# Kernel tuning notes

Measured on AMD Instinct MI355X. Metric: run time of the kernel, lower is better.

The kernel has to match this reference:

```python
import jax, jax.numpy as jnp
import numpy as np

B, K, D_MODEL = 64, 256, 512
D_STATE, D_CONV, EXPAND = 16, 4, 1
D_INNER = EXPAND * D_MODEL
DT_RANK = (D_MODEL + 15) // 16  # 32
EPS = 1e-5


def _layer_norm(x, g, b):
    m = jnp.mean(x, axis=-1, keepdims=True)
    v = jnp.mean(jnp.square(x - m), axis=-1, keepdims=True)
    return (x - m) * jax.lax.rsqrt(v + EPS) * g + b


def _silu(x):
    return x * jax.nn.sigmoid(x)


def _mamba_block(x, in_proj_w, conv_w, conv_b, x_proj_w, dt_proj_w, dt_proj_b, A_log, Dp, out_proj_w):
    # x: (B, K, d_model)
    b, k, _ = x.shape
    d_inner = A_log.shape[0]
    d_state = A_log.shape[1]
    dt_rank = dt_proj_w.shape[1]
    xz = x @ in_proj_w.T                      # (B, K, 2*d_inner)
    xi, z = jnp.split(xz, 2, axis=-1)
    # causal depthwise conv1d, width d_conv
    pad = conv_w.shape[1] - 1
    xp = jnp.pad(xi, ((0, 0), (pad, 0), (0, 0)))
    xc = conv_b + sum(xp[:, w:w + k, :] * conv_w[:, w] for w in range(conv_w.shape[1]))
    xc = _silu(xc)
    proj = xc @ x_proj_w.T                    # (B, K, dt_rank + 2*d_state)
    dtr = proj[..., :dt_rank]
    Bc = proj[..., dt_rank:dt_rank + d_state]  # (B, K, d_state)
    Cc = proj[..., dt_rank + d_state:]         # (B, K, d_state)
    dt = jax.nn.softplus(dtr @ dt_proj_w.T + dt_proj_b)  # (B, K, d_inner)
    A = -jnp.exp(A_log)                       # (d_inner, d_state)

    def step(h, inp):
        dt_t, x_t, B_t, C_t = inp             # (B,d_inner),(B,d_inner),(B,d_state),(B,d_state)
        dA = jnp.exp(dt_t[:, :, None] * A)    # (B, d_inner, d_state)
        h = dA * h + (dt_t * x_t)[:, :, None] * B_t[:, None, :]
        y = jnp.einsum('bds,bs->bd', h, C_t)
        return h, y

    h0 = jnp.zeros((b, d_inner, d_state), x.dtype)
    xs = (dt.transpose(1, 0, 2), xc.transpose(1, 0, 2),
          Bc.transpose(1, 0, 2), Cc.transpose(1, 0, 2))
    _, ys = jax.lax.scan(step, h0, xs)        # ys: (K, B, d_inner)
    y = ys.transpose(1, 0, 2) + xc * Dp       # skip term D*x
    y = y * _silu(z)
    return y @ out_proj_w.T


def setup_inputs() -> dict:
    key = jax.random.key(0)
    ks = jax.random.split(key, 8)
    s = 0.02
    slots = jax.random.normal(ks[0], (B, K, D_MODEL), dtype=jnp.float32)
    in_proj_w = jax.random.normal(ks[1], (2 * D_INNER, D_MODEL), jnp.float32) * s
    conv_w = jax.random.normal(ks[2], (D_INNER, D_CONV), jnp.float32) * 0.1
    conv_b = jnp.zeros((D_INNER,), jnp.float32)
    x_proj_w = jax.random.normal(ks[3], (DT_RANK + 2 * D_STATE, D_INNER), jnp.float32) * s
    dt_proj_w = jax.random.normal(ks[4], (D_INNER, DT_RANK), jnp.float32) * s
    dt_proj_b = jax.random.normal(ks[5], (D_INNER,), jnp.float32) * 0.1 - 4.0  # small softplus(dt)
    A_log = jnp.log(jnp.broadcast_to(jnp.arange(1, D_STATE + 1, dtype=jnp.float32), (D_INNER, D_STATE)))
    Dp = jnp.ones((D_INNER,), jnp.float32)
    out_proj_w = jax.random.normal(ks[6], (D_MODEL, D_INNER), jnp.float32) * s
    ln_g = jnp.ones((D_MODEL,), jnp.float32)
    ln_b = jnp.zeros((D_MODEL,), jnp.float32)
    fln_g = jnp.ones((D_MODEL,), jnp.float32)
    fln_b = jnp.zeros((D_MODEL,), jnp.float32)
    return {"slots": slots, "ln_g": ln_g, "ln_b": ln_b,
            "in_proj_w": in_proj_w, "conv_w": conv_w, "conv_b": conv_b,
            "x_proj_w": x_proj_w, "dt_proj_w": dt_proj_w, "dt_proj_b": dt_proj_b,
            "A_log": A_log, "Dp": Dp, "out_proj_w": out_proj_w,
            "fln_g": fln_g, "fln_b": fln_b}


def reference(slots, ln_g, ln_b, in_proj_w, conv_w, conv_b, x_proj_w,
              dt_proj_w, dt_proj_b, A_log, Dp, out_proj_w, fln_g, fln_b):
    x = slots
    # num_layers = 1: pre-norm -> mamba -> residual
    residual = x
    x = _layer_norm(x, ln_g, ln_b)
    x = _mamba_block(x, in_proj_w, conv_w, conv_b, x_proj_w,
                     dt_proj_w, dt_proj_b, A_log, Dp, out_proj_w)
    x = x + residual
    return _layer_norm(x, fln_g, fln_b)
```

## Files before the change

### kernel.cpp

```cpp
#include <hip/hip_runtime.h>
#include <hip/hip_bf16.h>


#define NTOK 16384
#define DM   512

typedef __attribute__((ext_vector_type(8))) short bf16x8;
typedef __attribute__((ext_vector_type(4))) float f32x4;

__device__ __forceinline__ unsigned short f2bf(float f){
  unsigned int u = __float_as_uint(f);
  u = (u + 0x7fffu + ((u >> 16) & 1u)) >> 16;
  return (unsigned short)u;
}
__device__ __forceinline__ float bfu(unsigned short p){ return __uint_as_float(((unsigned int)p) << 16); }
__device__ __forceinline__ unsigned int pk2(float a, float b){
  return (unsigned int)f2bf(a) | ((unsigned int)f2bf(b) << 16);
}
__device__ __forceinline__ float silu(float a){ return a / (1.f + __expf(-a)); }

__device__ __forceinline__ float qsum(float x){
  x += __int_as_float(__builtin_amdgcn_mov_dpp(__float_as_int(x), 0xB1, 0xF, 0xF, true));
  x += __int_as_float(__builtin_amdgcn_mov_dpp(__float_as_int(x), 0x4E, 0xF, 0xF, true));
  return x;
}

__device__ __forceinline__ void async_cp16(const unsigned short* g, unsigned short* l){
  __builtin_amdgcn_global_load_lds(
      (const __attribute__((address_space(1))) unsigned int*)g,
      (__attribute__((address_space(3))) unsigned int*)l, 16, 0, 0);
}

__global__ __launch_bounds__(256) void k_cvtw(const float* __restrict__ W,
                                              unsigned short* __restrict__ Wb){
  int i = (blockIdx.x*256 + threadIdx.x)*8;
  float4 a = *(const float4*)(W+i);
  float4 b = *(const float4*)(W+i+4);
  uint4 st = { pk2(a.x,a.y), pk2(a.z,a.w), pk2(b.x,b.y), pk2(b.z,b.w) };
  *(uint4*)(Wb+i) = st;
}

__global__ __launch_bounds__(64) void k_ln(const float* __restrict__ x,
                                           const float* __restrict__ g,
                                           const float* __restrict__ b,
                                           unsigned short* __restrict__ out){
  int tok  = blockIdx.x;
  int lane = threadIdx.x;
  const float* row = x + (size_t)tok*DM + lane*8;
  float4 r0 = *(const float4*)row;
  float4 r1 = *(const float4*)(row + 4);
  float v[8] = {r0.x,r0.y,r0.z,r0.w, r1.x,r1.y,r1.z,r1.w};
  float s = 0.f;
  #pragma unroll
  for (int i=0;i<8;i++) s += v[i];
  #pragma unroll
  for (int o=32;o;o>>=1) s += __shfl_xor(s, o, 64);
  float m = s * (1.0f/512.0f);
  float vs = 0.f;
  #pragma unroll
  for (int i=0;i<8;i++){ float d = v[i]-m; vs += d*d; }
  #pragma unroll
  for (int o=32;o;o>>=1) vs += __shfl_xor(vs, o, 64);
  float rs = rsqrtf(vs*(1.0f/512.0f) + 1e-5f);
  float4 g0 = *(const float4*)(g + lane*8);
  float4 g1 = *(const float4*)(g + lane*8 + 4);
  float4 b0 = *(const float4*)(b + lane*8);
  float4 b1 = *(const float4*)(b + lane*8 + 4);
  float gv[8] = {g0.x,g0.y,g0.z,g0.w, g1.x,g1.y,g1.z,g1.w};
  float bv[8] = {b0.x,b0.y,b0.z,b0.w, b1.x,b1.y,b1.z,b1.w};
  float o8[8];
  #pragma unroll
  for (int i=0;i<8;i++) o8[i] = (v[i]-m)*rs*gv[i] + bv[i];
  uint4 st = { pk2(o8[0],o8[1]), pk2(o8[2],o8[3]), pk2(o8[4],o8[5]), pk2(o8[6],o8[7]) };
  *(uint4*)(out + (size_t)tok*DM + lane*8) = st;
}

__global__ __launch_bounds__(256) void k_gemm(const unsigned short* __restrict__ A,
                                              const unsigned short* __restrict__ Wb,
                                              float* __restrict__ out_f,
                                              unsigned short* __restrict__ out_b,
                                              unsigned short* __restrict__ out_x,
                                              int mode){
  __shared__ unsigned short As[2][128*32];
  __shared__ unsigned short Bs[2][128*32];
  int t0  = blockIdx.x * 128;
  int n0  = blockIdx.y * 128;
  int tid = threadIdx.x;
  int lane = tid & 63;
  int wv  = tid >> 6;
  int mw  = wv & 1, nw = wv >> 1;
  int m15 = lane & 15, quad = lane >> 4;

  int srow   = wv*32 + (lane >> 2);
  int schunk = ((lane & 3) ^ ((lane >> 3) & 3)) * 8;
  const unsigned short* gA = A  + (size_t)(t0 + srow)*DM + schunk;
  const unsigned short* gB = Wb + (size_t)(n0 + srow)*DM + schunk;
  unsigned short* asb0 = &As[0][(wv*32)*32];
  unsigned short* bsb0 = &Bs[0][(wv*32)*32];
  unsigned short* asb1 = &As[1][(wv*32)*32];
  unsigned short* bsb1 = &Bs[1][(wv*32)*32];

  async_cp16(gA,         asb0);
  async_cp16(gA + 16*DM, asb0 + 16*32);
  async_cp16(gB,         bsb0);
  async_cp16(gB + 16*DM, bsb0 + 16*32);

  f32x4 acc[4][4];
  #pragma unroll
  for (int rb=0;rb<4;rb++)
    #pragma unroll
    for (int cb=0;cb<4;cb++) acc[rb][cb] = (f32x4){0.f,0.f,0.f,0.f};

  int rdsw = (quad ^ ((m15 >> 1) & 3)) * 8;
  int cur = 0;
  for (int ks = 0; ks < 16; ks++){
    __syncthreads();
    if (ks < 15){
      const unsigned short* nA = gA + (ks+1)*32;
      const unsigned short* nB = gB + (ks+1)*32;
      unsigned short* na = cur ? asb0 : asb1;
      unsigned short* nb = cur ? bsb0 : bsb1;
      async_cp16(nA,         na);
      async_cp16(nA + 16*DM, na + 16*32);
      async_cp16(nB,         nb);
      async_cp16(nB + 16*DM, nb + 16*32);
    }
    bf16x8 af[4], bfr[4];
    #pragma unroll
    for (int rb=0;rb<4;rb++)
      af[rb] = *(const bf16x8*)&As[cur][(mw*64 + rb*16 + m15)*32 + rdsw];
    #pragma unroll
    for (int cb=0;cb<4;cb++)
      bfr[cb] = *(const bf16x8*)&Bs[cur][(nw*64 + cb*16 + m15)*32 + rdsw];
    #pragma unroll
    for (int rb=0;rb<4;rb++)
      #pragma unroll
      for (int cb=0;cb<4;cb++)
        acc[rb][cb] = __builtin_amdgcn_mfma_f32_16x16x32_bf16(af[rb], bfr[cb], acc[rb][cb], 0, 0, 0);
    cur ^= 1;
  }

  #pragma unroll
  for (int rb=0;rb<4;rb++){
    int tok0 = t0 + mw*64 + rb*16 + quad*4;
    int b    = tok0 >> 8;
    int tl0  = tok0 & 255;
    #pragma unroll
    for (int cb=0;cb<4;cb++){
      int nn = n0 + nw*64 + cb*16 + m15;
      f32x4 v = acc[rb][cb];
      if (mode == 0){
        if (nn < DM){
          *(uint2*)(out_x + ((size_t)(b*DM + nn))*256 + tl0)
              = (uint2){ pk2(v[0],v[1]), pk2(v[2],v[3]) };
        } else {
          *(uint2*)(out_b + ((size_t)(b*DM + (nn - DM)))*256 + tl0)
              = (uint2){ pk2(silu(v[0]), silu(v[1])), pk2(silu(v[2]), silu(v[3])) };
        }
      } else {
        #pragma unroll
        for (int r=0;r<4;r++) out_f[(size_t)(tok0+r)*DM + nn] = v[r];
      }
    }
  }
}

__global__ __launch_bounds__(256) void k_xproj(const unsigned short* __restrict__ xiTb,
                                               const float* __restrict__ cw,
                                               const float* __restrict__ cb,
                                               const unsigned short* __restrict__ xpwb,
                                               const unsigned short* __restrict__ dtwb,
                                               const float* __restrict__ dtb,
                                               unsigned short* __restrict__ dtTb,
                                               unsigned short* __restrict__ xcT,
                                               float* __restrict__ Bc,
                                               float* __restrict__ Cc){
  __shared__ unsigned short xcb[16*520];
  __shared__ unsigned short pjA[16*40];
  int t0  = blockIdx.x * 16;
  int b   = t0 >> 8;
  int tl0 = t0 & 255;
  int tid = threadIdx.x;
  int lane = tid & 63;
  int wv  = tid >> 6;
  int m15 = lane & 15, quad = lane >> 4;

  #pragma unroll
  for (int j=0;j<2;j++){
    int d = tid + 256*j;
    float4 cr = *(const float4*)(cw + d*4);
    float a0 = cb[d];
    const unsigned short* row = xiTb + ((size_t)(b*DM + d))*256;
    float w[20];
    if (tl0 == 0){
      w[0]=w[1]=w[2]=w[3]=0.f;
      #pragma unroll
      for (int q2=0;q2<4;q2++){
        uint2 v2 = *(const uint2*)(row + q2*4);
        w[4+q2*4+0]=bfu((unsigned short)v2.x);
        w[4+q2*4+1]=bfu((unsigned short)(v2.x>>16));
        w[4+q2*4+2]=bfu((unsigned short)v2.y);
        w[4+q2*4+3]=bfu((unsigned short)(v2.y>>16));
      }
    } else {
      const unsigned short* p = row + tl0 - 4;
      #pragma unroll
      for (int q2=0;q2<5;q2++){
        uint2 v2 = *(const uint2*)(p + q2*4);
        w[q2*4+0]=bfu((unsigned short)v2.x);
        w[q2*4+1]=bfu((unsigned short)(v2.x>>16));
        w[q2*4+2]=bfu((unsigned short)v2.y);
        w[q2*4+3]=bfu((unsigned short)(v2.y>>16));
      }
    }
    unsigned int pkv[8];
    #pragma unroll
    for (int t=0;t<16;t+=2){
      float s0 = silu(a0 + w[t+1]*cr.x + w[t+2]*cr.y + w[t+3]*cr.z + w[t+4]*cr.w);
      float s1 = silu(a0 + w[t+2]*cr.x + w[t+3]*cr.y + w[t+4]*cr.z + w[t+5]*cr.w);
      unsigned int pp = pk2(s0, s1);
      xcb[t*520 + d]     = (unsigned short)pp;
      xcb[(t+1)*520 + d] = (unsigned short)(pp >> 16);
      pkv[t>>1] = pp;
    }
    unsigned short* xr = xcT + ((size_t)(b*DM + d))*256 + tl0;
    *(uint4*)(xr)     = (uint4){ pkv[0], pkv[1], pkv[2], pkv[3] };
    *(uint4*)(xr + 8) = (uint4){ pkv[4], pkv[5], pkv[6], pkv[7] };
  }
  __syncthreads();

  f32x4 pacc = (f32x4){0.f,0.f,0.f,0.f};
  #pragma unroll 4
  for (int ks=0; ks<16; ks++){
    bf16x8 af  = *(const bf16x8*)&xcb[m15*520 + ks*32 + quad*8];
    bf16x8 bfr = *(const bf16x8*)(xpwb + (size_t)(wv*16 + m15)*DM + ks*32 + quad*8);
    pacc = __builtin_amdgcn_mfma_f32_16x16x32_bf16(af, bfr, pacc, 0, 0, 0);
  }

  if (wv < 2){
    #pragma unroll
    for (int r=0;r<4;r++)
      pjA[(quad*4 + r)*40 + wv*16 + m15] = f2bf(pacc[r]);
  } else if (wv == 2){
    #pragma unroll
    for (int r=0;r<4;r++)
      Bc[(size_t)(t0 + quad*4 + r)*16 + m15] = pacc[r];
  } else {
    #pragma unroll
    for (int r=0;r<4;r++)
      Cc[(size_t)(t0 + quad*4 + r)*16 + m15] = pacc[r];
  }
  __syncthreads();

  bf16x8 adt = *(const bf16x8*)&pjA[m15*40 + quad*8];
  #pragma unroll
  for (int j2=0;j2<8;j2++){
    int nn = (wv*8 + j2)*16 + m15;
    bf16x8 bfr = *(const bf16x8*)(dtwb + nn*32 + quad*8);
    f32x4 dacc = (f32x4){0.f,0.f,0.f,0.f};
    dacc = __builtin_amdgcn_mfma_f32_16x16x32_bf16(adt, bfr, dacc, 0, 0, 0);
    float bb = dtb[nn];
    float s0 = dacc[0] + bb, s1 = dacc[1] + bb, s2 = dacc[2] + bb, s3 = dacc[3] + bb;
    float o0 = (s0 > 20.f) ? s0 : log1pf(__expf(s0));
    float o1 = (s1 > 20.f) ? s1 : log1pf(__expf(s1));
    float o2 = (s2 > 20.f) ? s2 : log1pf(__expf(s2));
    float o3 = (s3 > 20.f) ? s3 : log1pf(__expf(s3));
    *(uint2*)(dtTb + ((size_t)(b*DM + nn))*256 + tl0 + quad*4)
        = (uint2){ pk2(o0,o1), pk2(o2,o3) };
  }
}

#define SCAN_STEP(DV, UV, BV, CV, ZS, OUT) do {                                 \
    float dv_ = (DV);                                                           \
    float u_  = (UV);                                                           \
    float du_ = dv_*u_;                                                         \
    h0 = fmaf(exp2f(dv_*A0), h0, du_*(BV).x);                                   \
    h1 = fmaf(exp2f(dv_*A1), h1, du_*(BV).y);                                   \
    h2 = fmaf(exp2f(dv_*A2), h2, du_*(BV).z);                                   \
    h3 = fmaf(exp2f(dv_*A3), h3, du_*(BV).w);                                   \
    float yy_ = fmaf(h3,(CV).w, fmaf(h2,(CV).z, fmaf(h1,(CV).y, h0*(CV).x)));   \
    yy_ = qsum(yy_);                                                            \
    OUT = fmaf(u_, Dv, yy_) * (ZS);                                             \
  } while(0)

#define SCAN_LOAD(DD, UU, ZZ, B0,B1,B2,B3, C0,C1,C2,C3) do {                    \
    DD  = *(const uint2*)dtp;  UU = *(const uint2*)xup;                         \
    ZZ  = *(const uint2*)zsp;                                                   \
    B0 = *(const float4*)(Bp);    B1 = *(const float4*)(Bp+16);                 \
    B2 = *(const float4*)(Bp+32); B3 = *(const float4*)(Bp+48);                 \
    C0 = *(const float4*)(Cp);    C1 = *(const float4*)(Cp+16);                 \
    C2 = *(const float4*)(Cp+32); C3 = *(const float4*)(Cp+48);                 \
    dtp += 4; xup += 4; zsp += 4; Bp += 64; Cp += 64;                           \
  } while(0)

#define SCAN_BODY(DD, UU, ZZ, B0,B1,B2,B3, C0,C1,C2,C3) do {                    \
    float dv0_ = __uint_as_float((DD).x << 16);                                 \
    float dv1_ = __uint_as_float((DD).x & 0xffff0000u);                         \
    float dv2_ = __uint_as_float((DD).y << 16);                                 \
    float dv3_ = __uint_as_float((DD).y & 0xffff0000u);                         \
    float u0_ = __uint_as_float((UU).x << 16);                                  \
    float u1_ = __uint_as_float((UU).x & 0xffff0000u);                          \
    float u2_ = __uint_as_float((UU).y << 16);                                  \
    float u3_ = __uint_as_float((UU).y & 0xffff0000u);                          \
    float zs0_ = __uint_as_float((ZZ).x << 16);                                 \
    float zs1_ = __uint_as_float((ZZ).x & 0xffff0000u);                         \
    float zs2_ = __uint_as_float((ZZ).y << 16);                                 \
    float zs3_ = __uint_as_float((ZZ).y & 0xffff0000u);                         \
    float o0_,o1_,o2_,o3_;                                                      \
    SCAN_STEP(dv0_,u0_,B0,C0,zs0_,o0_);                                         \
    SCAN_STEP(dv1_,u1_,B1,C1,zs1_,o1_);                                         \
    SCAN_STEP(dv2_,u2_,B2,C2,zs2_,o2_);                                         \
    SCAN_STEP(dv3_,u3_,B3,C3,zs3_,o3_);                                         \
    float osel_ = (sl==0)?o0_:(sl==1)?o1_:(sl==2)?o2_:o3_;                      \
    *yo = f2bf(osel_);                                                          \
    yo += 4*DM;                                                                 \
  } while(0)

__global__ __launch_bounds__(256) void k_scan(const unsigned short* __restrict__ dtT,
                                              const unsigned short* __restrict__ xcT,
                                              const unsigned short* __restrict__ zsT,
                                              const float* __restrict__ Bc,
                                              const float* __restrict__ Cc,
                                              const float* __restrict__ Alog,
                                              const float* __restrict__ Dpw,
                                              unsigned short* __restrict__ ya){
  int tid = threadIdx.x;
  int sl  = tid & 3;
  int q   = blockIdx.x*64 + (tid >> 2);
  int d   = q & 511;
  int b   = q >> 9;
  const float LOG2E = 1.44269504f;
  float4 Alr = *(const float4*)(Alog + d*16 + sl*4);
  float A0 = -__expf(Alr.x)*LOG2E, A1 = -__expf(Alr.y)*LOG2E;
  float A2 = -__expf(Alr.z)*LOG2E, A3 = -__expf(Alr.w)*LOG2E;
  float Dv = Dpw[d];
  float h0=0.f, h1=0.f, h2=0.f, h3=0.f;
  const unsigned short* dtp = dtT + (size_t)q*256;
  const unsigned short* xup = xcT + (size_t)q*256;
  const unsigned short* zsp = zsT + (size_t)q*256;
  unsigned short* yo = ya + (size_t)b*256*DM + d + sl*DM;
  const float* Bp = Bc + (size_t)b*4096 + sl*4;
  const float* Cp = Cc + (size_t)b*4096 + sl*4;

  uint2 ddA, uuA, zzA; float4 a0,a1,a2,a3, e0,e1,e2,e3;
  uint2 ddB, uuB, zzB; float4 f0,f1,f2,f3, g0,g1,g2,g3;

  SCAN_LOAD(ddA,uuA,zzA, a0,a1,a2,a3, e0,e1,e2,e3);
  for (int it = 0; it < 64; it += 2){
    SCAN_LOAD(ddB,uuB,zzB, f0,f1,f2,f3, g0,g1,g2,g3);
    SCAN_BODY(ddA,uuA,zzA, a0,a1,a2,a3, e0,e1,e2,e3);
    if (it < 62)
      SCAN_LOAD(ddA,uuA,zzA, a0,a1,a2,a3, e0,e1,e2,e3);
    SCAN_BODY(ddB,uuB,zzB, f0,f1,f2,f3, g0,g1,g2,g3);
  }
}

__global__ __launch_bounds__(64) void k_fln(const float* __restrict__ o,
                                            const float* __restrict__ resid,
                                            const float* __restrict__ g,
                                            const float* __restrict__ b,
                                            float* __restrict__ out){
  int tok  = blockIdx.x;
  int lane = threadIdx.x;
  const float* row = o     + (size_t)tok*DM + lane*8;
  const float* rr  = resid + (size_t)tok*DM + lane*8;
  float4 r0 = *(const float4*)row;
  float4 r1 = *(const float4*)(row + 4);
  float4 s0 = *(const float4*)rr;
  float4 s1 = *(const float4*)(rr + 4);
  float v[8] = {r0.x+s0.x, r0.y+s0.y, r0.z+s0.z, r0.w+s0.w,
                r1.x+s1.x, r1.y+s1.y, r1.z+s1.z, r1.w+s1.w};
  float s = 0.f;
  #pragma unroll
  for (int i=0;i<8;i++) s += v[i];
  #pragma unroll
  for (int o2=32;o2;o2>>=1) s += __shfl_xor(s, o2, 64);
  float m = s * (1.0f/512.0f);
  float vs = 0.f;
  #pragma unroll
  for (int i=0;i<8;i++){ float d = v[i]-m; vs += d*d; }
  #pragma unroll
  for (int o2=32;o2;o2>>=1) vs += __shfl_xor(vs, o2, 64);
  float rs = rsqrtf(vs*(1.0f/512.0f) + 1e-5f);
  float4 g0 = *(const float4*)(g + lane*8);
  float4 g1 = *(const float4*)(g + lane*8 + 4);
  float4 b0 = *(const float4*)(b + lane*8);
  float4 b1 = *(const float4*)(b + lane*8 + 4);
  float gv[8] = {g0.x,g0.y,g0.z,g0.w, g1.x,g1.y,g1.z,g1.w};
  float bv[8] = {b0.x,b0.y,b0.z,b0.w, b1.x,b1.y,b1.z,b1.w};
  float o8[8];
  #pragma unroll
  for (int i=0;i<8;i++) o8[i] = (v[i]-m)*rs*gv[i] + bv[i];
  float4* op = (float4*)(out + (size_t)tok*DM + lane*8);
  op[0] = make_float4(o8[0],o8[1],o8[2],o8[3]);
  op[1] = make_float4(o8[4],o8[5],o8[6],o8[7]);
}

extern "C" void kernel_launch(void* const* d_in, const int* in_sizes, int n_in,
                              void* d_out, int out_size, void* d_ws, size_t ws_size,
                              hipStream_t stream) {
  const float* slots     = (const float*)d_in[0];
  const float* ln_g      = (const float*)d_in[1];
  const float* ln_b      = (const float*)d_in[2];
  const float* in_proj_w = (const float*)d_in[3];
  const float* conv_w    = (const float*)d_in[4];
  const float* conv_b    = (const float*)d_in[5];
  const float* x_proj_w  = (const float*)d_in[6];
  const float* dt_proj_w = (const float*)d_in[7];
  const float* dt_proj_b = (const float*)d_in[8];
  const float* A_log     = (const float*)d_in[9];
  const float* Dp        = (const float*)d_in[10];
  const float* out_projw = (const float*)d_in[11];
  const float* fln_g     = (const float*)d_in[12];
  const float* fln_b     = (const float*)d_in[13];
  float* out = (float*)d_out;

  const size_t MB = 1024*1024;
  char* base = (char*)d_ws;
  unsigned short* xiTb = (unsigned short*)(base);
  unsigned short* xlnb = (unsigned short*)(base + 32*MB);
  unsigned short* yab  = xlnb;
  unsigned short* xpwb = xlnb;
  unsigned short* dtwb = xlnb + 32768;
  unsigned short* zsT  = (unsigned short*)(base + 48*MB);
  unsigned short* WbO  = zsT;
  unsigned short* dtTb = (unsigned short*)(base + 64*MB);
  unsigned short* xcT  = (unsigned short*)(base + 80*MB);
  float*          dto  = (float*)(base + 64*MB);
  unsigned short* WbI  = (unsigned short*)dto;
  float*          Bc   = (float*)(base + 96*MB);
  float*          Cc   = (float*)(base + 97*MB);

  k_ln   <<<NTOK,           64, 0, stream>>>(slots, ln_g, ln_b, xlnb);
  k_cvtw <<<256,           256, 0, stream>>>(in_proj_w, WbI);
  k_gemm <<<dim3(128, 8),  256, 0, stream>>>(xlnb, WbI, (float*)0, zsT, xiTb, 0);
  k_cvtw <<<16,            256, 0, stream>>>(x_proj_w, xpwb);
  k_cvtw <<<8,             256, 0, stream>>>(dt_proj_w, dtwb);
  k_xproj<<<NTOK/16,       256, 0, stream>>>(xiTb, conv_w, conv_b, xpwb, dtwb, dt_proj_b,
                                             dtTb, xcT, Bc, Cc);
  k_scan <<<512,           256, 0, stream>>>(dtTb, xcT, zsT, Bc, Cc, A_log, Dp, yab);
  k_cvtw <<<128,           256, 0, stream>>>(out_projw, WbO);
  k_gemm <<<dim3(128, 4),  256, 0, stream>>>(yab, WbO, dto, (unsigned short*)0, (unsigned short*)0, 1);
  k_fln  <<<NTOK,           64, 0, stream>>>(dto, slots, fln_g, fln_b, out);
}
```

Before: 294.8 us.

## Split causal conv into own kernel with row-major xi/xc layout

The in_proj GEMM now writes the xi half row-major (token x channel) instead of transposed. A new k_conv kernel computes the causal conv plus SiLU along time with a sliding register window and writes row-major xc. k_xproj then loads xc tiles into swizzled shared memory with async 16-byte copies, and k_scan reads xc row-major one element per step. This is meant to replace the transposed strided stores and the redundant halo reloads with coalesced traffic. The cost is an extra kernel launch, an extra round trip of xc through memory, and scalar 2-byte loads in the scan.

```diff
diff --git a/kernel.cpp b/kernel.cpp
--- a/kernel.cpp
+++ b/kernel.cpp
@@ -151,8 +151,8 @@
       f32x4 v = acc[rb][cb];
       if (mode == 0){
         if (nn < DM){
-          *(uint2*)(out_x + ((size_t)(b*DM + nn))*256 + tl0)
-              = (uint2){ pk2(v[0],v[1]), pk2(v[2],v[3]) };
+          #pragma unroll
+          for (int r=0;r<4;r++) out_x[(size_t)(tok0+r)*DM + nn] = f2bf(v[r]);
         } else {
           *(uint2*)(out_b + ((size_t)(b*DM + (nn - DM)))*256 + tl0)
               = (uint2){ pk2(silu(v[0]), silu(v[1])), pk2(silu(v[2]), silu(v[3])) };
@@ -165,17 +165,49 @@
   }
 }
 
-__global__ __launch_bounds__(256) void k_xproj(const unsigned short* __restrict__ xiTb,
-                                               const float* __restrict__ cw,
-                                               const float* __restrict__ cb,
+__global__ __launch_bounds__(256) void k_conv(const unsigned short* __restrict__ xiR,
+                                              const float* __restrict__ cw,
+                                              const float* __restrict__ cb,
+                                              unsigned short* __restrict__ xcR){
+  int bb = blockIdx.x >> 3;
+  int tc = blockIdx.x & 7;
+  int d2 = threadIdx.x * 2;
+  int gt0 = bb*256 + tc*32;
+  const unsigned short* rp = xiR + (size_t)gt0*DM + d2;
+  unsigned short*       op = xcR + (size_t)gt0*DM + d2;
+  float4 cwa = *(const float4*)(cw + d2*4);
+  float4 cwb = *(const float4*)(cw + d2*4 + 4);
+  float cba = cb[d2], cbb = cb[d2+1];
+  float a1,a2,a3, b1,b2,b3;
+  if (tc == 0){
+    a1=a2=a3=0.f; b1=b2=b3=0.f;
+  } else {
+    unsigned int h1 = *(const unsigned int*)(rp - 1*DM);
+    unsigned int h2 = *(const unsigned int*)(rp - 2*DM);
+    unsigned int h3 = *(const unsigned int*)(rp - 3*DM);
+    a1 = bfu((unsigned short)h1); b1 = bfu((unsigned short)(h1>>16));
+    a2 = bfu((unsigned short)h2); b2 = bfu((unsigned short)(h2>>16));
+    a3 = bfu((unsigned short)h3); b3 = bfu((unsigned short)(h3>>16));
+  }
+  #pragma unroll 8
+  for (int t=0;t<32;t++){
+    unsigned int v = *(const unsigned int*)(rp + (size_t)t*DM);
+    float xa = bfu((unsigned short)v), xb = bfu((unsigned short)(v>>16));
+    float sa = silu(cba + a3*cwa.x + a2*cwa.y + a1*cwa.z + xa*cwa.w);
+    float sb = silu(cbb + b3*cwb.x + b2*cwb.y + b1*cwb.z + xb*cwb.w);
+    *(unsigned int*)(op + (size_t)t*DM) = pk2(sa, sb);
+    a3=a2; a2=a1; a1=xa;  b3=b2; b2=b1; b1=xb;
+  }
+}
+
+__global__ __launch_bounds__(256) void k_xproj(const unsigned short* __restrict__ xcR,
                                                const unsigned short* __restrict__ xpwb,
                                                const unsigned short* __restrict__ dtwb,
                                                const float* __restrict__ dtb,
                                                unsigned short* __restrict__ dtTb,
-                                               unsigned short* __restrict__ xcT,
                                                float* __restrict__ Bc,
                                                float* __restrict__ Cc){
-  __shared__ unsigned short xcb[16*520];
+  __shared__ unsigned short xcs[16*512];
   __shared__ unsigned short pjA[16*40];
   int t0  = blockIdx.x * 16;
   int b   = t0 >> 8;
@@ -185,54 +217,20 @@
   int wv  = tid >> 6;
   int m15 = lane & 15, quad = lane >> 4;
 
-  #pragma unroll
-  for (int j=0;j<2;j++){
-    int d = tid + 256*j;
-    float4 cr = *(const float4*)(cw + d*4);
-    float a0 = cb[d];
-    const unsigned short* row = xiTb + ((size_t)(b*DM + d))*256;
-    float w[20];
-    if (tl0 == 0){
-      w[0]=w[1]=w[2]=w[3]=0.f;
-      #pragma unroll
-      for (int q2=0;q2<4;q2++){
-        uint2 v2 = *(const uint2*)(row + q2*4);
-        w[4+q2*4+0]=bfu((unsigned short)v2.x);
-        w[4+q2*4+1]=bfu((unsigned short)(v2.x>>16));
-        w[4+q2*4+2]=bfu((unsigned short)v2.y);
-        w[4+q2*4+3]=bfu((unsigned short)(v2.y>>16));
-      }
-    } else {
-      const unsigned short* p = row + tl0 - 4;
-      #pragma unroll
-      for (int q2=0;q2<5;q2++){
-        uint2 v2 = *(const uint2*)(p + q2*4);
-        w[q2*4+0]=bfu((unsigned short)v2.x);
-        w[q2*4+1]=bfu((unsigned short)(v2.x>>16));
-        w[q2*4+2]=bfu((unsigned short)v2.y);
-        w[q2*4+3]=bfu((unsigned short)(v2.y>>16));
-      }
-    }
-    unsigned int pkv[8];
-    #pragma unroll
-    for (int t=0;t<16;t+=2){
-      float s0 = silu(a0 + w[t+1]*cr.x + w[t+2]*cr.y + w[t+3]*cr.z + w[t+4]*cr.w);
-      float s1 = silu(a0 + w[t+2]*cr.x + w[t+3]*cr.y + w[t+4]*cr.z + w[t+5]*cr.w);
-      unsigned int pp = pk2(s0, s1);
-      xcb[t*520 + d]     = (unsigned short)pp;
-      xcb[(t+1)*520 + d] = (unsigned short)(pp >> 16);
-      pkv[t>>1] = pp;
-    }
-    unsigned short* xr = xcT + ((size_t)(b*DM + d))*256 + tl0;
-    *(uint4*)(xr)     = (uint4){ pkv[0], pkv[1], pkv[2], pkv[3] };
-    *(uint4*)(xr + 8) = (uint4){ pkv[4], pkv[5], pkv[6], pkv[7] };
+  int srow   = lane >> 2;
+  int schunk = ((lane & 3) ^ ((lane >> 3) & 3)) * 8;
+  #pragma unroll
+  for (int k2=0;k2<4;k2++){
+    int ks = wv*4 + k2;
+    async_cp16(xcR + (size_t)(t0 + srow)*DM + ks*32 + schunk, &xcs[ks*512]);
   }
   __syncthreads();
 
+  int rdsw = (quad ^ ((m15 >> 1) & 3)) * 8;
   f32x4 pacc = (f32x4){0.f,0.f,0.f,0.f};
   #pragma unroll 4
   for (int ks=0; ks<16; ks++){
-    bf16x8 af  = *(const bf16x8*)&xcb[m15*520 + ks*32 + quad*8];
+    bf16x8 af  = *(const bf16x8*)&xcs[ks*512 + m15*32 + rdsw];
     bf16x8 bfr = *(const bf16x8*)(xpwb + (size_t)(wv*16 + m15)*DM + ks*32 + quad*8);
     pacc = __builtin_amdgcn_mfma_f32_16x16x32_bf16(af, bfr, pacc, 0, 0, 0);
   }
@@ -283,41 +281,37 @@
     OUT = fmaf(u_, Dv, yy_) * (ZS);                                             \
   } while(0)
 
-#define SCAN_LOAD(DD, UU, ZZ, B0,B1,B2,B3, C0,C1,C2,C3) do {                    \
-    DD  = *(const uint2*)dtp;  UU = *(const uint2*)xup;                         \
-    ZZ  = *(const uint2*)zsp;                                                   \
+#define SCAN_LOAD(DD, ZZ, U0,U1,U2,U3, B0,B1,B2,B3, C0,C1,C2,C3) do {           \
+    DD  = *(const uint2*)dtp;  ZZ = *(const uint2*)zsp;                         \
+    U0 = xur[0]; U1 = xur[DM]; U2 = xur[2*DM]; U3 = xur[3*DM];                  \
     B0 = *(const float4*)(Bp);    B1 = *(const float4*)(Bp+16);                 \
     B2 = *(const float4*)(Bp+32); B3 = *(const float4*)(Bp+48);                 \
     C0 = *(const float4*)(Cp);    C1 = *(const float4*)(Cp+16);                 \
     C2 = *(const float4*)(Cp+32); C3 = *(const float4*)(Cp+48);                 \
-    dtp += 4; xup += 4; zsp += 4; Bp += 64; Cp += 64;                           \
+    dtp += 4; zsp += 4; xur += 4*DM; Bp += 64; Cp += 64;                        \
   } while(0)
 
-#define SCAN_BODY(DD, UU, ZZ, B0,B1,B2,B3, C0,C1,C2,C3) do {                    \
+#define SCAN_BODY(DD, ZZ, U0,U1,U2,U3, B0,B1,B2,B3, C0,C1,C2,C3) do {           \
     float dv0_ = __uint_as_float((DD).x << 16);                                 \
     float dv1_ = __uint_as_float((DD).x & 0xffff0000u);                         \
     float dv2_ = __uint_as_float((DD).y << 16);                                 \
     float dv3_ = __uint_as_float((DD).y & 0xffff0000u);                         \
-    float u0_ = __uint_as_float((UU).x << 16);                                  \
-    float u1_ = __uint_as_float((UU).x & 0xffff0000u);                          \
-    float u2_ = __uint_as_float((UU).y << 16);                                  \
-    float u3_ = __uint_as_float((UU).y & 0xffff0000u);                          \
     float zs0_ = __uint_as_float((ZZ).x << 16);                                 \
     float zs1_ = __uint_as_float((ZZ).x & 0xffff0000u);                         \
     float zs2_ = __uint_as_float((ZZ).y << 16);                                 \
     float zs3_ = __uint_as_float((ZZ).y & 0xffff0000u);                         \
     float o0_,o1_,o2_,o3_;                                                      \
-    SCAN_STEP(dv0_,u0_,B0,C0,zs0_,o0_);                                         \
-    SCAN_STEP(dv1_,u1_,B1,C1,zs1_,o1_);                                         \
-    SCAN_STEP(dv2_,u2_,B2,C2,zs2_,o2_);                                         \
-    SCAN_STEP(dv3_,u3_,B3,C3,zs3_,o3_);                                         \
+    SCAN_STEP(dv0_,bfu(U0),B0,C0,zs0_,o0_);                                     \
+    SCAN_STEP(dv1_,bfu(U1),B1,C1,zs1_,o1_);                                     \
+    SCAN_STEP(dv2_,bfu(U2),B2,C2,zs2_,o2_);                                     \
+    SCAN_STEP(dv3_,bfu(U3),B3,C3,zs3_,o3_);                                     \
     float osel_ = (sl==0)?o0_:(sl==1)?o1_:(sl==2)?o2_:o3_;                      \
     *yo = f2bf(osel_);                                                          \
     yo += 4*DM;                                                                 \
   } while(0)
 
 __global__ __launch_bounds__(256) void k_scan(const unsigned short* __restrict__ dtT,
-                                              const unsigned short* __restrict__ xcT,
+                                              const unsigned short* __restrict__ xcR,
                                               const unsigned short* __restrict__ zsT,
                                               const float* __restrict__ Bc,
                                               const float* __restrict__ Cc,
@@ -336,22 +330,22 @@
   float Dv = Dpw[d];
   float h0=0.f, h1=0.f, h2=0.f, h3=0.f;
   const unsigned short* dtp = dtT + (size_t)q*256;
-  const unsigned short* xup = xcT + (size_t)q*256;
   const unsigned short* zsp = zsT + (size_t)q*256;
+  const unsigned short* xur = xcR + (size_t)(b*256)*DM + d;
   unsigned short* yo = ya + (size_t)b*256*DM + d + sl*DM;
   const float* Bp = Bc + (size_t)b*4096 + sl*4;
   const float* Cp = Cc + (size_t)b*4096 + sl*4;
 
-  uint2 ddA, uuA, zzA; float4 a0,a1,a2,a3, e0,e1,e2,e3;
-  uint2 ddB, uuB, zzB; float4 f0,f1,f2,f3, g0,g1,g2,g3;
-
-  SCAN_LOAD(ddA,uuA,zzA, a0,a1,a2,a3, e0,e1,e2,e3);
+  uint2 ddA, zzA; unsigned short uA0,uA1,uA2,uA3; float4 a0,a1,a2,a3, e0,e1,e2,e3;
+  uint2 ddB, zzB; unsigned short uB0,uB1,uB2,uB3; float4 f0,f1,f2,f3, g0,g1,g2,g3;
+
+  SCAN_LOAD(ddA,zzA, uA0,uA1,uA2,uA3, a0,a1,a2,a3, e0,e1,e2,e3);
   for (int it = 0; it < 64; it += 2){
-    SCAN_LOAD(ddB,uuB,zzB, f0,f1,f2,f3, g0,g1,g2,g3);
-    SCAN_BODY(ddA,uuA,zzA, a0,a1,a2,a3, e0,e1,e2,e3);
+    SCAN_LOAD(ddB,zzB, uB0,uB1,uB2,uB3, f0,f1,f2,f3, g0,g1,g2,g3);
+    SCAN_BODY(ddA,zzA, uA0,uA1,uA2,uA3, a0,a1,a2,a3, e0,e1,e2,e3);
     if (it < 62)
-      SCAN_LOAD(ddA,uuA,zzA, a0,a1,a2,a3, e0,e1,e2,e3);
-    SCAN_BODY(ddB,uuB,zzB, f0,f1,f2,f3, g0,g1,g2,g3);
+      SCAN_LOAD(ddA,zzA, uA0,uA1,uA2,uA3, a0,a1,a2,a3, e0,e1,e2,e3);
+    SCAN_BODY(ddB,zzB, uB0,uB1,uB2,uB3, f0,f1,f2,f3, g0,g1,g2,g3);
   }
 }
 
@@ -417,7 +411,7 @@
 
   const size_t MB = 1024*1024;
   char* base = (char*)d_ws;
-  unsigned short* xiTb = (unsigned short*)(base);
+  unsigned short* xiR  = (unsigned short*)(base);
   unsigned short* xlnb = (unsigned short*)(base + 32*MB);
   unsigned short* yab  = xlnb;
   unsigned short* xpwb = xlnb;
@@ -425,7 +419,7 @@
   unsigned short* zsT  = (unsigned short*)(base + 48*MB);
   unsigned short* WbO  = zsT;
   unsigned short* dtTb = (unsigned short*)(base + 64*MB);
-  unsigned short* xcT  = (unsigned short*)(base + 80*MB);
+  unsigned short* xcR  = (unsigned short*)(base + 80*MB);
   float*          dto  = (float*)(base + 64*MB);
   unsigned short* WbI  = (unsigned short*)dto;
   float*          Bc   = (float*)(base + 96*MB);
@@ -433,12 +427,13 @@
 
   k_ln   <<<NTOK,           64, 0, stream>>>(slots, ln_g, ln_b, xlnb);
   k_cvtw <<<256,           256, 0, stream>>>(in_proj_w, WbI);
-  k_gemm <<<dim3(128, 8),  256, 0, stream>>>(xlnb, WbI, (float*)0, zsT, xiTb, 0);
+  k_gemm <<<dim3(128, 8),  256, 0, stream>>>(xlnb, WbI, (float*)0, zsT, xiR, 0);
   k_cvtw <<<16,            256, 0, stream>>>(x_proj_w, xpwb);
   k_cvtw <<<8,             256, 0, stream>>>(dt_proj_w, dtwb);
-  k_xproj<<<NTOK/16,       256, 0, stream>>>(xiTb, conv_w, conv_b, xpwb, dtwb, dt_proj_b,
-                                             dtTb, xcT, Bc, Cc);
-  k_scan <<<512,           256, 0, stream>>>(dtTb, xcT, zsT, Bc, Cc, A_log, Dp, yab);
+  k_conv <<<512,           256, 0, stream>>>(xiR, conv_w, conv_b, xcR);
+  k_xproj<<<NTOK/16,       256, 0, stream>>>(xcR, xpwb, dtwb, dt_proj_b,
+                                             dtTb, Bc, Cc);
+  k_scan <<<512,           256, 0, stream>>>(dtTb, xcR, zsT, Bc, Cc, A_log, Dp, yab);
   k_cvtw <<<128,           256, 0, stream>>>(out_projw, WbO);
   k_gemm <<<dim3(128, 4),  256, 0, stream>>>(yab, WbO, dto, (unsigned short*)0, (unsigned short*)0, 1);
   k_fln  <<<NTOK,           64, 0, stream>>>(dto, slots, fln_g, fln_b, out);
```

New measurement: 276.7 us. 1.07x faster.
